# Performance work log

Hardware: AMD Instinct MI355X
Metric: run time of the kernel (lower is better)

The kernel has to match this reference:

```python
import jax, jax.numpy as jnp
import numpy as np

B, D, H, S = 4096, 512, 512, 16
EVENT_THRESH = 0.85  # hard-coded in original forward (e_t > 0.85), tau unused


def setup_inputs() -> dict:
    key = jax.random.key(0)
    ks = jax.random.split(key, 17)
    s = 0.02
    return {
        "x_t": jax.random.normal(ks[0], (B, D), jnp.float32),
        "h_lstm": jax.random.normal(ks[1], (B, H), jnp.float32),
        "c_lstm": jax.random.normal(ks[2], (B, H), jnp.float32),
        "slots": jax.random.normal(ks[3], (B, S, D), jnp.float32),
        "ptr": jax.random.randint(ks[4], (B,), 0, S, jnp.int32),
        # SequenceMemoryCell params
        "value_W": jax.random.normal(ks[5], (D, D), jnp.float32) * s,
        "value_b": jnp.zeros((D,), jnp.float32),
        "ed_W": jax.random.normal(ks[6], (1, D), jnp.float32) * s,
        "ed_b": jnp.zeros((1,), jnp.float32),
        "pos_emb": jax.random.normal(ks[7], (S, D), jnp.float32),
        "lstm_Wih": jax.random.normal(ks[8], (4 * H, D), jnp.float32) * s,
        "lstm_Whh": jax.random.normal(ks[9], (4 * H, H), jnp.float32) * s,
        "lstm_bih": jnp.zeros((4 * H,), jnp.float32),
        "lstm_bhh": jnp.zeros((4 * H,), jnp.float32),
        # outer hand-written LSTM params
        "Wih": jax.random.normal(ks[10], (4 * H, D + H), jnp.float32) * s,
        "bih": jnp.zeros((4 * H,), jnp.float32),
        "Whh": jax.random.normal(ks[11], (4 * H, H), jnp.float32) * s,
    }


def reference(x_t, h_lstm, c_lstm, slots, value_W, value_b, ed_W, ed_b,
              pos_emb, lstm_Wih, lstm_Whh, lstm_bih, lstm_bhh,
              Wih, bih, Whh, ptr):
    b, n_slots, d = slots.shape
    h = lstm_Whh.shape[1]
    # --- SequenceMemoryCell ---
    e_t = jax.nn.sigmoid(x_t @ ed_W.T + ed_b)            # (B, 1)
    event = e_t > EVENT_THRESH                            # (B, 1) bool
    v = x_t @ value_W.T + value_b                         # (B, D)
    # conditional pointer-indexed write into circular slot buffer
    write = (jnp.arange(n_slots)[None, :] == ptr[:, None]) & event  # (B, S)
    new_slots = jnp.where(write[:, :, None], v[:, None, :], slots)
    new_ptr = (ptr + event[:, 0].astype(ptr.dtype)) % n_slots
    slots_pe = new_slots + pos_emb[None, :, :]            # (B, S, D)
    # slot-fuser LSTM over n_slots (PyTorch gate order i,f,g,o), h0=c0=0
    def step(carry, x_s):
        hh, cc = carry
        g = x_s @ lstm_Wih.T + lstm_bih + hh @ lstm_Whh.T + lstm_bhh
        i, f, gg, o = jnp.split(g, 4, axis=1)
        cc = jax.nn.sigmoid(f) * cc + jax.nn.sigmoid(i) * jnp.tanh(gg)
        hh = jax.nn.sigmoid(o) * jnp.tanh(cc)
        return (hh, cc), None
    h0 = jnp.zeros((b, h), slots.dtype)
    (h_mem, _), _ = jax.lax.scan(step, (h0, h0), jnp.swapaxes(slots_pe, 0, 1))
    # --- outer hand-written LSTM cell on [x_t; h_mem] ---
    gates = jnp.concatenate([x_t, h_mem], axis=1) @ Wih.T + bih + h_lstm @ Whh.T
    i, f, g_t, o = jnp.split(gates, 4, axis=1)
    c_new = jax.nn.sigmoid(f) * c_lstm + jax.nn.sigmoid(i) * jnp.tanh(g_t)
    h_new = jax.nn.sigmoid(o) * jnp.tanh(c_new)
    return (h_new, c_new, h_mem, new_slots, new_ptr)
```

## Files before the change

### kernel.cpp

```cpp
#include <hip/hip_runtime.h>
#include <hip/hip_bf16.h>

constexpr int kB = 4096;
constexpr int kD = 512;
constexpr int kH = 512;
constexpr int kS = 16;
constexpr int kG = 2048;
constexpr int kChainBlocks = 1024;

typedef __attribute__((ext_vector_type(8))) short bf16x8_t;
typedef __attribute__((ext_vector_type(4))) float f32x4_t;

__device__ __forceinline__ short f2bf(float x) {
  __hip_bfloat16 h = __float2bfloat16(x);
  return *reinterpret_cast<short*>(&h);
}
__device__ __forceinline__ float sigm(float x) { return 1.0f / (1.0f + expf(-x)); }

__device__ __forceinline__ int swz(int row, int kElem) {
  return row * 64 + (((kElem >> 3) ^ (row & 7)) << 3);
}

__global__ void bar_init_kernel(unsigned* __restrict__ ctr, int n)
{
  int i = blockIdx.x * blockDim.x + threadIdx.x;
  if (i < n) ctr[i] = 0u;
}

__global__ void event_kernel(const float* __restrict__ x,
                             const float* __restrict__ edW,
                             const float* __restrict__ edb,
                             const int* __restrict__ ptr,
                             int* __restrict__ ev,
                             float* __restrict__ newptr_out)
{
  int b = blockIdx.x * 4 + (threadIdx.x >> 6);
  int lane = threadIdx.x & 63;
  const float* xr = x + (size_t)b * kD;
  float sum = 0.f;
  for (int k = lane; k < kD; k += 64) sum += xr[k] * edW[k];
  #pragma unroll
  for (int off = 32; off; off >>= 1) sum += __shfl_down(sum, off, 64);
  if (lane == 0) {
    float e = sigm(sum + edb[0]);
    int evt = (e > 0.85f) ? 1 : 0;
    ev[b] = evt;
    newptr_out[b] = (float)((ptr[b] + evt) & (kS - 1));
  }
}

__global__ void f2b_kernel(const float* __restrict__ src, short* __restrict__ dst, int n4)
{
  int i = blockIdx.x * blockDim.x + threadIdx.x;
  if (i >= n4) return;
  const float4 v = reinterpret_cast<const float4*>(src)[i];
  short4 o;
  o.x = f2bf(v.x); o.y = f2bf(v.y); o.z = f2bf(v.z); o.w = f2bf(v.w);
  reinterpret_cast<short4*>(dst)[i] = o;
}

__global__ void packw_gates_kernel(const float* __restrict__ W1, int w1,
                                   const float* __restrict__ W2, int w2,
                                   short* __restrict__ dst, int total4)
{
  int i = blockIdx.x * blockDim.x + threadIdx.x;
  if (i >= total4) return;
  long e = (long)i * 4;
  int K = w1 + w2;
  long p = e / K;
  int col = (int)(e - p * K);
  long r = (long)(((p >> 4) & 3) * 512 + ((p >> 6) << 4) + (p & 15));
  const float* src = (col < w1) ? (W1 + r * (long)w1 + col)
                                : (W2 + r * (long)w2 + (col - w1));
  const float4 v = *reinterpret_cast<const float4*>(src);
  short4 o; o.x=f2bf(v.x); o.y=f2bf(v.y); o.z=f2bf(v.z); o.w=f2bf(v.w);
  *reinterpret_cast<short4*>(dst + e) = o;
}

__global__ void packbias_kernel(const float* __restrict__ b1, const float* __restrict__ b2,
                                float* __restrict__ o, int n)
{
  int p = blockIdx.x * blockDim.x + threadIdx.x;
  if (p >= n) return;
  int r = ((p >> 4) & 3) * 512 + ((p >> 6) << 4) + (p & 15);
  float v = b1[r];
  if (b2) v += b2[r];
  o[p] = v;
}

__global__ void slot_update_kernel(const float* __restrict__ slots,
                                   const float* __restrict__ v,
                                   const float* __restrict__ pos_emb,
                                   const int* __restrict__ ptr,
                                   const int* __restrict__ ev,
                                   float* __restrict__ new_slots,
                                   short* __restrict__ slots_pe)
{
  size_t i = (size_t)blockIdx.x * blockDim.x + threadIdx.x;
  size_t e = i * 4;
  int d = (int)(e & (kD - 1));
  size_t bs = e >> 9;
  int s = (int)(bs & (kS - 1));
  size_t b = bs >> 4;
  float4 val;
  if (ev[b] && (ptr[b] == s)) val = *reinterpret_cast<const float4*>(v + (b << 9) + d);
  else                        val = *reinterpret_cast<const float4*>(slots + e);
  *reinterpret_cast<float4*>(new_slots + e) = val;
  const float4 pe = *reinterpret_cast<const float4*>(pos_emb + ((size_t)s << 9) + d);
  short4 o;
  o.x = f2bf(val.x + pe.x); o.y = f2bf(val.y + pe.y);
  o.z = f2bf(val.z + pe.z); o.w = f2bf(val.w + pe.w);
  *reinterpret_cast<short4*>(slots_pe + e) = o;
}

__global__ __launch_bounds__(256, 4)
void chain_kernel(const short* __restrict__ slots_pe,
                  const short* __restrict__ W,
                  const float* __restrict__ bias,
                  short* __restrict__ hsteps,
                  float* __restrict__ hmem,
                  unsigned* __restrict__ barrier_ctr)
{
  __shared__ short As[128 * 64];
  __shared__ short Ws[64 * 64];
  const int tid  = threadIdx.x;
  const int wave = tid >> 6;
  const int lane = tid & 63;

  const int vid = (blockIdx.x & 7) * 128 + (blockIdx.x >> 3);
  const int bx  = vid >> 5;
  const int by  = vid & 31;
  const int row0 = bx * 128;
  const int col0 = by * 64;

  const int srow   = tid >> 3;
  const int scol   = (tid & 7) * 8;
  const int schunk = (((tid >> 3) ^ tid) & 7) * 8;

  float bv[4];
  #pragma unroll
  for (int n = 0; n < 4; ++n)
    bv[n] = bias[col0 + n * 16 + (lane & 15)];
  const int hcol = by * 16 + (lane & 15);

  float c_reg[2][4];
  #pragma unroll
  for (int m = 0; m < 2; ++m)
    #pragma unroll
    for (int r = 0; r < 4; ++r) c_reg[m][r] = 0.f;

  for (int s = 0; s < kS; ++s) {
    f32x4_t acc[2][4];
    #pragma unroll
    for (int m = 0; m < 2; ++m)
      #pragma unroll
      for (int n = 0; n < 4; ++n) acc[m][n] = {0.f, 0.f, 0.f, 0.f};

    const short* A = slots_pe + (size_t)s * kD;
    for (int k0 = 0; k0 < 512; k0 += 64) {
      __syncthreads();
      #pragma unroll
      for (int j = 0; j < 4; ++j) {
        const int arow = j * 32 + srow;
        const short* asrc = A + (size_t)(row0 + arow) * (kS * kD) + k0 + schunk;
        __builtin_amdgcn_global_load_lds(
            (const __attribute__((address_space(1))) void*)asrc,
            (__attribute__((address_space(3))) void*)&As[arow * 64 + scol], 16, 0, 0);
      }
      #pragma unroll
      for (int j = 0; j < 2; ++j) {
        const int wrow = j * 32 + srow;
        const short* wsrc = W + (size_t)(col0 + wrow) * 1024 + k0 + schunk;
        __builtin_amdgcn_global_load_lds(
            (const __attribute__((address_space(1))) void*)wsrc,
            (__attribute__((address_space(3))) void*)&Ws[wrow * 64 + scol], 16, 0, 0);
      }
      __syncthreads();
      #pragma unroll
      for (int kk = 0; kk < 64; kk += 32) {
        bf16x8_t af[2], bfr[4];
        const int kcol = kk + (lane >> 4) * 8;
        const int ar = wave * 32 + (lane & 15);
        const int br = lane & 15;
        #pragma unroll
        for (int m = 0; m < 2; ++m)
          af[m] = *reinterpret_cast<const bf16x8_t*>(&As[swz(ar + m * 16, kcol)]);
        #pragma unroll
        for (int n = 0; n < 4; ++n)
          bfr[n] = *reinterpret_cast<const bf16x8_t*>(&Ws[swz(br + n * 16, kcol)]);
        #pragma unroll
        for (int m = 0; m < 2; ++m)
          #pragma unroll
          for (int n = 0; n < 4; ++n)
            acc[m][n] = __builtin_amdgcn_mfma_f32_16x16x32_bf16(af[m], bfr[n], acc[m][n], 0, 0, 0);
      }
    }

    if (s > 0) {
      const short* Hp = hsteps + (size_t)(s - 1) * kB * kH;
      unsigned* ctr = barrier_ctr + (((s - 1) * 32 + bx) << 4);
      __syncthreads();
      if (tid == 0) {
        __hip_atomic_fetch_add(ctr, 1u, __ATOMIC_RELAXED, __HIP_MEMORY_SCOPE_AGENT);
        while (__hip_atomic_load(ctr, __ATOMIC_RELAXED, __HIP_MEMORY_SCOPE_AGENT) < 32u)
          __builtin_amdgcn_s_sleep(2);
      }
      __syncthreads();
      for (int k0 = 0; k0 < 512; k0 += 64) {
        __syncthreads();
        #pragma unroll
        for (int j = 0; j < 4; ++j) {
          const int arow = j * 32 + srow;
          const short* asrc = Hp + (size_t)(row0 + arow) * kH + k0 + schunk;
          __builtin_amdgcn_global_load_lds(
              (const __attribute__((address_space(1))) void*)asrc,
              (__attribute__((address_space(3))) void*)&As[arow * 64 + scol], 16, 0, 0);
        }
        #pragma unroll
        for (int j = 0; j < 2; ++j) {
          const int wrow = j * 32 + srow;
          const short* wsrc = W + (size_t)(col0 + wrow) * 1024 + 512 + k0 + schunk;
          __builtin_amdgcn_global_load_lds(
              (const __attribute__((address_space(1))) void*)wsrc,
              (__attribute__((address_space(3))) void*)&Ws[wrow * 64 + scol], 16, 0, 0);
        }
        __syncthreads();
        #pragma unroll
        for (int kk = 0; kk < 64; kk += 32) {
          bf16x8_t af[2], bfr[4];
          const int kcol = kk + (lane >> 4) * 8;
          const int ar = wave * 32 + (lane & 15);
          const int br = lane & 15;
          #pragma unroll
          for (int m = 0; m < 2; ++m)
            af[m] = *reinterpret_cast<const bf16x8_t*>(&As[swz(ar + m * 16, kcol)]);
          #pragma unroll
          for (int n = 0; n < 4; ++n)
            bfr[n] = *reinterpret_cast<const bf16x8_t*>(&Ws[swz(br + n * 16, kcol)]);
          #pragma unroll
          for (int m = 0; m < 2; ++m)
            #pragma unroll
            for (int n = 0; n < 4; ++n)
              acc[m][n] = __builtin_amdgcn_mfma_f32_16x16x32_bf16(af[m], bfr[n], acc[m][n], 0, 0, 0);
        }
      }
    }

    short* Hout = hsteps + (size_t)s * kB * kH;
    #pragma unroll
    for (int m = 0; m < 2; ++m) {
      const int rbase = row0 + wave * 32 + m * 16 + (lane >> 4) * 4;
      #pragma unroll
      for (int r = 0; r < 4; ++r) {
        const size_t idx = (size_t)(rbase + r) * kH + hcol;
        const float gi = acc[m][0][r] + bv[0];
        const float gf = acc[m][1][r] + bv[1];
        const float gg = acc[m][2][r] + bv[2];
        const float go = acc[m][3][r] + bv[3];
        const float cn = sigm(gf) * c_reg[m][r] + sigm(gi) * tanhf(gg);
        const float hn = sigm(go) * tanhf(cn);
        c_reg[m][r] = cn;
        Hout[idx] = f2bf(hn);
        if (s == kS - 1) hmem[idx] = hn;
      }
    }
  }
}

__global__ __launch_bounds__(256, 4)
void gemm_fused_kernel(const short* __restrict__ A0, int lda0,
                       const short* __restrict__ A1, int lda1,
                       const short* __restrict__ A2, int lda2,
                       int nseg, const short* __restrict__ W, int ldw,
                       const float* __restrict__ bias, int mode, int nby,
                       float* __restrict__ C, int ldc,
                       const float* __restrict__ c_in,
                       float* __restrict__ h_out, float* __restrict__ c_out)
{
  __shared__ short As[128 * 64];
  __shared__ short Ws[64 * 64];
  const int tid  = threadIdx.x;
  const int wave = tid >> 6;
  const int lane = tid & 63;

  const int nb  = gridDim.x;
  const int vid = (blockIdx.x & 7) * (nb >> 3) + (blockIdx.x >> 3);
  const int bx  = vid / nby;
  const int by  = vid - bx * nby;
  const int row0 = bx * 128;
  const int col0 = by * 64;
  const int K = nseg << 9;

  f32x4_t acc[2][4];
  #pragma unroll
  for (int m = 0; m < 2; ++m)
    #pragma unroll
    for (int n = 0; n < 4; ++n)
      acc[m][n] = {0.f, 0.f, 0.f, 0.f};

  const int srow   = tid >> 3;
  const int scol   = (tid & 7) * 8;
  const int schunk = (((tid >> 3) ^ tid) & 7) * 8;

  for (int k0 = 0; k0 < K; k0 += 64) {
    const int seg = k0 >> 9;
    const int ks  = k0 & 511;
    const short* Ap = (seg == 0) ? A0 : ((seg == 1) ? A1 : A2);
    const int   lda = (seg == 0) ? lda0 : ((seg == 1) ? lda1 : lda2);
    __syncthreads();
    #pragma unroll
    for (int j = 0; j < 4; ++j) {
      const int arow = j * 32 + srow;
      const short* asrc = Ap + (size_t)(row0 + arow) * lda + ks + schunk;
      __builtin_amdgcn_global_load_lds(
          (const __attribute__((address_space(1))) void*)asrc,
          (__attribute__((address_space(3))) void*)&As[arow * 64 + scol], 16, 0, 0);
    }
    #pragma unroll
    for (int j = 0; j < 2; ++j) {
      const int wrow = j * 32 + srow;
      const short* wsrc = W + (size_t)(col0 + wrow) * ldw + k0 + schunk;
      __builtin_amdgcn_global_load_lds(
          (const __attribute__((address_space(1))) void*)wsrc,
          (__attribute__((address_space(3))) void*)&Ws[wrow * 64 + scol], 16, 0, 0);
    }
    __syncthreads();
    #pragma unroll
    for (int kk = 0; kk < 64; kk += 32) {
      bf16x8_t af[2], bfr[4];
      const int kcol = kk + (lane >> 4) * 8;
      const int ar = wave * 32 + (lane & 15);
      const int br = lane & 15;
      #pragma unroll
      for (int m = 0; m < 2; ++m)
        af[m] = *reinterpret_cast<const bf16x8_t*>(&As[swz(ar + m * 16, kcol)]);
      #pragma unroll
      for (int n = 0; n < 4; ++n)
        bfr[n] = *reinterpret_cast<const bf16x8_t*>(&Ws[swz(br + n * 16, kcol)]);
      #pragma unroll
      for (int m = 0; m < 2; ++m)
        #pragma unroll
        for (int n = 0; n < 4; ++n)
          acc[m][n] = __builtin_amdgcn_mfma_f32_16x16x32_bf16(af[m], bfr[n], acc[m][n], 0, 0, 0);
    }
  }

  float bv[4];
  #pragma unroll
  for (int n = 0; n < 4; ++n)
    bv[n] = bias[col0 + n * 16 + (lane & 15)];

  if (mode == 0) {
    #pragma unroll
    for (int n = 0; n < 4; ++n) {
      const int col = col0 + n * 16 + (lane & 15);
      #pragma unroll
      for (int m = 0; m < 2; ++m) {
        const int rbase = row0 + wave * 32 + m * 16 + (lane >> 4) * 4;
        #pragma unroll
        for (int r = 0; r < 4; ++r)
          C[(size_t)(rbase + r) * ldc + col] = acc[m][n][r] + bv[n];
      }
    }
    return;
  }

  const int hcol = (col0 >> 6) * 16 + (lane & 15);
  #pragma unroll
  for (int m = 0; m < 2; ++m) {
    const int rbase = row0 + wave * 32 + m * 16 + (lane >> 4) * 4;
    #pragma unroll
    for (int r = 0; r < 4; ++r) {
      const size_t idx = (size_t)(rbase + r) * kH + hcol;
      const float gi = acc[m][0][r] + bv[0];
      const float gf = acc[m][1][r] + bv[1];
      const float gg = acc[m][2][r] + bv[2];
      const float go = acc[m][3][r] + bv[3];
      const float cn = sigm(gf) * c_in[idx] + sigm(gi) * tanhf(gg);
      const float hn = sigm(go) * tanhf(cn);
      c_out[idx] = cn;
      h_out[idx] = hn;
    }
  }
}

extern "C" void kernel_launch(void* const* d_in, const int* in_sizes, int n_in,
                              void* d_out, int out_size, void* d_ws, size_t ws_size,
                              hipStream_t stream)
{
  const float* x_t      = (const float*)d_in[0];
  const float* h_lstm   = (const float*)d_in[1];
  const float* c_lstm   = (const float*)d_in[2];
  const float* slots    = (const float*)d_in[3];
  const int*   ptr      = (const int*)  d_in[4];
  const float* value_W  = (const float*)d_in[5];
  const float* value_b  = (const float*)d_in[6];
  const float* ed_W     = (const float*)d_in[7];
  const float* ed_b     = (const float*)d_in[8];
  const float* pos_emb  = (const float*)d_in[9];
  const float* lstm_Wih = (const float*)d_in[10];
  const float* lstm_Whh = (const float*)d_in[11];
  const float* lstm_bih = (const float*)d_in[12];
  const float* lstm_bhh = (const float*)d_in[13];
  const float* Wih      = (const float*)d_in[14];
  const float* bih      = (const float*)d_in[15];
  const float* Whh      = (const float*)d_in[16];

  float* out       = (float*)d_out;
  float* h_new     = out;
  float* c_new     = out + (size_t)kB * kH;
  float* h_mem     = out + (size_t)2 * kB * kH;
  float* new_slots = out + (size_t)3 * kB * kH;
  float* new_ptr   = out + (size_t)3 * kB * kH + (size_t)kB * kS * kD;

  char* ws = (char*)d_ws;
  size_t off = 0;
  auto alloc = [&](size_t bytes) { void* p = ws + off; off += (bytes + 255) & ~(size_t)255; return p; };
  int*      ev        = (int*)     alloc((size_t)kB * 4);
  unsigned* bar       = (unsigned*)alloc((size_t)15 * 32 * 16 * 4);
  short*    x_b       = (short*)   alloc((size_t)kB * kD * 2);
  short*    hlstm_b   = (short*)   alloc((size_t)kB * kH * 2);
  short*    vW_b      = (short*)   alloc((size_t)kD * kD * 2);
  short*    stepW_b   = (short*)   alloc((size_t)kG * (kD + kH) * 2);
  float*    stepBias  = (float*)   alloc((size_t)kG * 4);
  short*    outerW_b  = (short*)   alloc((size_t)kG * (kD + kH + kH) * 2);
  float*    outerBias = (float*)   alloc((size_t)kG * 4);
  float*    v_f32     = (float*)   alloc((size_t)kB * kD * 4);
  short*    hsteps    = (short*)   alloc((size_t)kS * kB * kH * 2);
  short*    slots_pe  = (short*)   alloc((size_t)kB * kS * kD * 2);
  (void)ws_size; (void)in_sizes; (void)n_in; (void)out_size;

  bar_init_kernel<<<(15 * 32 * 16 + 255) / 256, 256, 0, stream>>>(bar, 15 * 32 * 16);

  event_kernel<<<kB / 4, 256, 0, stream>>>(x_t, ed_W, ed_b, ptr, ev, new_ptr);

  f2b_kernel<<<(kB * kD / 4 + 255) / 256, 256, 0, stream>>>(x_t, x_b, kB * kD / 4);
  f2b_kernel<<<(kB * kH / 4 + 255) / 256, 256, 0, stream>>>(h_lstm, hlstm_b, kB * kH / 4);
  f2b_kernel<<<(kD * kD / 4 + 255) / 256, 256, 0, stream>>>(value_W, vW_b, kD * kD / 4);
  packw_gates_kernel<<<(kG * 1024 / 4 + 255) / 256, 256, 0, stream>>>(
      lstm_Wih, kD, lstm_Whh, kH, stepW_b, kG * 1024 / 4);
  packw_gates_kernel<<<(kG * 1536 / 4 + 255) / 256, 256, 0, stream>>>(
      Wih, kD + kH, Whh, kH, outerW_b, kG * 1536 / 4);
  packbias_kernel<<<(kG + 255) / 256, 256, 0, stream>>>(lstm_bih, lstm_bhh, stepBias, kG);
  packbias_kernel<<<(kG + 255) / 256, 256, 0, stream>>>(bih, nullptr, outerBias, kG);

  gemm_fused_kernel<<<(kB / 128) * (kD / 64), 256, 0, stream>>>(
      x_b, kD, nullptr, 0, nullptr, 0, 1, vW_b, kD, value_b, 0, kD / 64,
      v_f32, kD, nullptr, nullptr, nullptr);

  slot_update_kernel<<<(int)((size_t)kB * kS * kD / 4 / 256), 256, 0, stream>>>(
      slots, v_f32, pos_emb, ptr, ev, new_slots, slots_pe);

  chain_kernel<<<kChainBlocks, 256, 0, stream>>>(
      slots_pe, stepW_b, stepBias, hsteps, h_mem, bar);

  gemm_fused_kernel<<<(kB / 128) * (kG / 64), 256, 0, stream>>>(
      x_b, kD, hsteps + (size_t)(kS - 1) * kB * kH, kH, hlstm_b, kH, 3,
      outerW_b, kD + kH + kH, outerBias, 2, kG / 64,
      nullptr, 0, c_lstm, h_new, c_new);
}
```

Before: 817.3 us.

## Keep chain-kernel weight slice resident in LDS across all slot steps

The recurrent chain kernel now runs 256 persistent blocks of 512 threads. Each block loads its full 64-column weight slice (both input and recurrent halves, 128KB) into LDS once with a swizzled layout and keeps it there for all 16 steps. Activation fragments are read straight from global memory into registers instead of being staged through LDS, and each wave computes a 64x64 tile. This removes the per-step weight reloads and the per-k-chunk syncthreads, and the per-step barrier now uses release ordering on fewer counters. In exchange it runs fewer blocks with a large LDS footprint and relies on uncoalesced global loads for the A operand.

Measured after the change: 803.7 us. No clear change (-1.7%).

```diff
diff --git a/kernel.cpp b/kernel.cpp
--- a/kernel.cpp
+++ b/kernel.cpp
@@ -6,7 +6,7 @@
 constexpr int kH = 512;
 constexpr int kS = 16;
 constexpr int kG = 2048;
-constexpr int kChainBlocks = 1024;
+constexpr int kChainBlocks = 256;
 
 typedef __attribute__((ext_vector_type(8))) short bf16x8_t;
 typedef __attribute__((ext_vector_type(4))) float f32x4_t;
@@ -19,6 +19,9 @@
 
 __device__ __forceinline__ int swz(int row, int kElem) {
   return row * 64 + (((kElem >> 3) ^ (row & 7)) << 3);
+}
+__device__ __forceinline__ int wswz(int wrow, int kElem) {
+  return wrow * 1024 + ((((kElem >> 3) ^ wrow) & 7) << 3) + (kElem & ~63) ;
 }
 
 __global__ void bar_init_kernel(unsigned* __restrict__ ctr, int n)
@@ -113,7 +116,7 @@
   *reinterpret_cast<short4*>(slots_pe + e) = o;
 }
 
-__global__ __launch_bounds__(256, 4)
+__global__ __launch_bounds__(512, 2)
 void chain_kernel(const short* __restrict__ slots_pe,
                   const short* __restrict__ W,
                   const float* __restrict__ bias,
@@ -121,75 +124,67 @@
                   float* __restrict__ hmem,
                   unsigned* __restrict__ barrier_ctr)
 {
-  __shared__ short As[128 * 64];
-  __shared__ short Ws[64 * 64];
+  __shared__ short Wlds[64 * 1024];
   const int tid  = threadIdx.x;
   const int wave = tid >> 6;
   const int lane = tid & 63;
 
-  const int vid = (blockIdx.x & 7) * 128 + (blockIdx.x >> 3);
-  const int bx  = vid >> 5;
-  const int by  = vid & 31;
-  const int row0 = bx * 128;
+  const int bx  = blockIdx.x & 7;
+  const int by  = blockIdx.x >> 3;
+  const int row0 = bx * 512;
   const int col0 = by * 64;
 
-  const int srow   = tid >> 3;
-  const int scol   = (tid & 7) * 8;
-  const int schunk = (((tid >> 3) ^ tid) & 7) * 8;
+  #pragma unroll
+  for (int r8 = 0; r8 < 8; ++r8) {
+    const int wrow = r8 * 8 + wave;
+    #pragma unroll
+    for (int p = 0; p < 2; ++p) {
+      const int c = p * 64 + lane;
+      const short* src = W + (size_t)(col0 + wrow) * 1024 + ((c ^ (wrow & 7)) << 3);
+      __builtin_amdgcn_global_load_lds(
+          (const __attribute__((address_space(1))) void*)src,
+          (__attribute__((address_space(3))) void*)&Wlds[wrow * 1024 + p * 512],
+          16, 0, 0);
+    }
+  }
+  __syncthreads();
 
   float bv[4];
   #pragma unroll
   for (int n = 0; n < 4; ++n)
     bv[n] = bias[col0 + n * 16 + (lane & 15)];
   const int hcol = by * 16 + (lane & 15);
-
-  float c_reg[2][4];
-  #pragma unroll
-  for (int m = 0; m < 2; ++m)
+  const int rowsbase = row0 + wave * 64;
+  const int arow = rowsbase + (lane & 15);
+  const int klane = (lane >> 4) << 3;
+
+  float c_reg[4][4];
+  #pragma unroll
+  for (int m = 0; m < 4; ++m)
     #pragma unroll
     for (int r = 0; r < 4; ++r) c_reg[m][r] = 0.f;
 
   for (int s = 0; s < kS; ++s) {
-    f32x4_t acc[2][4];
-    #pragma unroll
-    for (int m = 0; m < 2; ++m)
+    f32x4_t acc[4][4];
+    #pragma unroll
+    for (int m = 0; m < 4; ++m)
       #pragma unroll
       for (int n = 0; n < 4; ++n) acc[m][n] = {0.f, 0.f, 0.f, 0.f};
 
-    const short* A = slots_pe + (size_t)s * kD;
-    for (int k0 = 0; k0 < 512; k0 += 64) {
-      __syncthreads();
-      #pragma unroll
-      for (int j = 0; j < 4; ++j) {
-        const int arow = j * 32 + srow;
-        const short* asrc = A + (size_t)(row0 + arow) * (kS * kD) + k0 + schunk;
-        __builtin_amdgcn_global_load_lds(
-            (const __attribute__((address_space(1))) void*)asrc,
-            (__attribute__((address_space(3))) void*)&As[arow * 64 + scol], 16, 0, 0);
-      }
-      #pragma unroll
-      for (int j = 0; j < 2; ++j) {
-        const int wrow = j * 32 + srow;
-        const short* wsrc = W + (size_t)(col0 + wrow) * 1024 + k0 + schunk;
-        __builtin_amdgcn_global_load_lds(
-            (const __attribute__((address_space(1))) void*)wsrc,
-            (__attribute__((address_space(3))) void*)&Ws[wrow * 64 + scol], 16, 0, 0);
-      }
-      __syncthreads();
-      #pragma unroll
-      for (int kk = 0; kk < 64; kk += 32) {
-        bf16x8_t af[2], bfr[4];
-        const int kcol = kk + (lane >> 4) * 8;
-        const int ar = wave * 32 + (lane & 15);
-        const int br = lane & 15;
-        #pragma unroll
-        for (int m = 0; m < 2; ++m)
-          af[m] = *reinterpret_cast<const bf16x8_t*>(&As[swz(ar + m * 16, kcol)]);
+    {
+      const short* Ap = slots_pe + (size_t)s * kD + (size_t)arow * (kS * kD);
+      #pragma unroll 4
+      for (int k0 = 0; k0 < 512; k0 += 32) {
+        const int kc = k0 + klane;
+        bf16x8_t af[4], bfr[4];
+        #pragma unroll
+        for (int m = 0; m < 4; ++m)
+          af[m] = *reinterpret_cast<const bf16x8_t*>(Ap + (size_t)(m * 16) * (kS * kD) + kc);
         #pragma unroll
         for (int n = 0; n < 4; ++n)
-          bfr[n] = *reinterpret_cast<const bf16x8_t*>(&Ws[swz(br + n * 16, kcol)]);
-        #pragma unroll
-        for (int m = 0; m < 2; ++m)
+          bfr[n] = *reinterpret_cast<const bf16x8_t*>(&Wlds[wswz((lane & 15) + n * 16, kc)]);
+        #pragma unroll
+        for (int m = 0; m < 4; ++m)
           #pragma unroll
           for (int n = 0; n < 4; ++n)
             acc[m][n] = __builtin_amdgcn_mfma_f32_16x16x32_bf16(af[m], bfr[n], acc[m][n], 0, 0, 0);
@@ -197,59 +192,37 @@
     }
 
     if (s > 0) {
-      const short* Hp = hsteps + (size_t)(s - 1) * kB * kH;
-      unsigned* ctr = barrier_ctr + (((s - 1) * 32 + bx) << 4);
+      unsigned* ctr = barrier_ctr + (((s - 1) * 8 + bx) << 4);
       __syncthreads();
       if (tid == 0) {
-        __hip_atomic_fetch_add(ctr, 1u, __ATOMIC_RELAXED, __HIP_MEMORY_SCOPE_AGENT);
+        __hip_atomic_fetch_add(ctr, 1u, __ATOMIC_RELEASE, __HIP_MEMORY_SCOPE_AGENT);
         while (__hip_atomic_load(ctr, __ATOMIC_RELAXED, __HIP_MEMORY_SCOPE_AGENT) < 32u)
           __builtin_amdgcn_s_sleep(2);
       }
       __syncthreads();
-      for (int k0 = 0; k0 < 512; k0 += 64) {
-        __syncthreads();
-        #pragma unroll
-        for (int j = 0; j < 4; ++j) {
-          const int arow = j * 32 + srow;
-          const short* asrc = Hp + (size_t)(row0 + arow) * kH + k0 + schunk;
-          __builtin_amdgcn_global_load_lds(
-              (const __attribute__((address_space(1))) void*)asrc,
-              (__attribute__((address_space(3))) void*)&As[arow * 64 + scol], 16, 0, 0);
-        }
-        #pragma unroll
-        for (int j = 0; j < 2; ++j) {
-          const int wrow = j * 32 + srow;
-          const short* wsrc = W + (size_t)(col0 + wrow) * 1024 + 512 + k0 + schunk;
-          __builtin_amdgcn_global_load_lds(
-              (const __attribute__((address_space(1))) void*)wsrc,
-              (__attribute__((address_space(3))) void*)&Ws[wrow * 64 + scol], 16, 0, 0);
-        }
-        __syncthreads();
-        #pragma unroll
-        for (int kk = 0; kk < 64; kk += 32) {
-          bf16x8_t af[2], bfr[4];
-          const int kcol = kk + (lane >> 4) * 8;
-          const int ar = wave * 32 + (lane & 15);
-          const int br = lane & 15;
-          #pragma unroll
-          for (int m = 0; m < 2; ++m)
-            af[m] = *reinterpret_cast<const bf16x8_t*>(&As[swz(ar + m * 16, kcol)]);
+      const short* Hp = hsteps + (size_t)(s - 1) * kB * kH + (size_t)arow * kH;
+      #pragma unroll 4
+      for (int k0 = 0; k0 < 512; k0 += 32) {
+        const int kc = k0 + klane;
+        bf16x8_t af[4], bfr[4];
+        #pragma unroll
+        for (int m = 0; m < 4; ++m)
+          af[m] = *reinterpret_cast<const bf16x8_t*>(Hp + (size_t)(m * 16) * kH + kc);
+        #pragma unroll
+        for (int n = 0; n < 4; ++n)
+          bfr[n] = *reinterpret_cast<const bf16x8_t*>(&Wlds[wswz((lane & 15) + n * 16, 512 + kc)]);
+        #pragma unroll
+        for (int m = 0; m < 4; ++m)
           #pragma unroll
           for (int n = 0; n < 4; ++n)
-            bfr[n] = *reinterpret_cast<const bf16x8_t*>(&Ws[swz(br + n * 16, kcol)]);
-          #pragma unroll
-          for (int m = 0; m < 2; ++m)
-            #pragma unroll
-            for (int n = 0; n < 4; ++n)
-              acc[m][n] = __builtin_amdgcn_mfma_f32_16x16x32_bf16(af[m], bfr[n], acc[m][n], 0, 0, 0);
-        }
+            acc[m][n] = __builtin_amdgcn_mfma_f32_16x16x32_bf16(af[m], bfr[n], acc[m][n], 0, 0, 0);
       }
     }
 
     short* Hout = hsteps + (size_t)s * kB * kH;
     #pragma unroll
-    for (int m = 0; m < 2; ++m) {
-      const int rbase = row0 + wave * 32 + m * 16 + (lane >> 4) * 4;
+    for (int m = 0; m < 4; ++m) {
+      const int rbase = rowsbase + m * 16 + (lane >> 4) * 4;
       #pragma unroll
       for (int r = 0; r < 4; ++r) {
         const size_t idx = (size_t)(rbase + r) * kH + hcol;
@@ -310,19 +283,19 @@
     __syncthreads();
     #pragma unroll
     for (int j = 0; j < 4; ++j) {
-      const int arow = j * 32 + srow;
-      const short* asrc = Ap + (size_t)(row0 + arow) * lda + ks + schunk;
+      const int r = j * 32 + srow;
+      const short* asrc = Ap + (size_t)(row0 + r) * lda + ks + schunk;
       __builtin_amdgcn_global_load_lds(
           (const __attribute__((address_space(1))) void*)asrc,
-          (__attribute__((address_space(3))) void*)&As[arow * 64 + scol], 16, 0, 0);
+          (__attribute__((address_space(3))) void*)&As[r * 64 + scol], 16, 0, 0);
     }
     #pragma unroll
     for (int j = 0; j < 2; ++j) {
-      const int wrow = j * 32 + srow;
-      const short* wsrc = W + (size_t)(col0 + wrow) * ldw + k0 + schunk;
+      const int r = j * 32 + srow;
+      const short* wsrc = W + (size_t)(col0 + r) * ldw + k0 + schunk;
       __builtin_amdgcn_global_load_lds(
           (const __attribute__((address_space(1))) void*)wsrc,
-          (__attribute__((address_space(3))) void*)&Ws[wrow * 64 + scol], 16, 0, 0);
+          (__attribute__((address_space(3))) void*)&Ws[r * 64 + scol], 16, 0, 0);
     }
     __syncthreads();
     #pragma unroll
@@ -417,7 +390,7 @@
   size_t off = 0;
   auto alloc = [&](size_t bytes) { void* p = ws + off; off += (bytes + 255) & ~(size_t)255; return p; };
   int*      ev        = (int*)     alloc((size_t)kB * 4);
-  unsigned* bar       = (unsigned*)alloc((size_t)15 * 32 * 16 * 4);
+  unsigned* bar       = (unsigned*)alloc((size_t)15 * 8 * 16 * 4);
   short*    x_b       = (short*)   alloc((size_t)kB * kD * 2);
   short*    hlstm_b   = (short*)   alloc((size_t)kB * kH * 2);
   short*    vW_b      = (short*)   alloc((size_t)kD * kD * 2);
@@ -430,7 +403,7 @@
   short*    slots_pe  = (short*)   alloc((size_t)kB * kS * kD * 2);
   (void)ws_size; (void)in_sizes; (void)n_in; (void)out_size;
 
-  bar_init_kernel<<<(15 * 32 * 16 + 255) / 256, 256, 0, stream>>>(bar, 15 * 32 * 16);
+  bar_init_kernel<<<(15 * 8 * 16 + 255) / 256, 256, 0, stream>>>(bar, 15 * 8 * 16);
 
   event_kernel<<<kB / 4, 256, 0, stream>>>(x_t, ed_W, ed_b, ptr, ev, new_ptr);
 
@@ -451,7 +424,7 @@
   slot_update_kernel<<<(int)((size_t)kB * kS * kD / 4 / 256), 256, 0, stream>>>(
       slots, v_f32, pos_emb, ptr, ev, new_slots, slots_pe);
 
-  chain_kernel<<<kChainBlocks, 256, 0, stream>>>(
+  chain_kernel<<<kChainBlocks, 512, 0, stream>>>(
       slots_pe, stepW_b, stepBias, hsteps, h_mem, bar);
 
   gemm_fused_kernel<<<(kB / 128) * (kG / 64), 256, 0, stream>>>(
```
